# Kernel tuning notes

Hardware: AMD Instinct MI355X
Metric: run time of the kernel (lower is better)

Reference implementation:

```python
import jax, jax.numpy as jnp
import numpy as np

EMBED_DIM = 512
N_HEADS = 16
HEAD_DIM = EMBED_DIM // N_HEADS  # 32


def setup_inputs() -> dict:
    key0 = jax.random.key(0)
    ks = jax.random.split(key0, 8)
    B, S, D = 4, 2048, EMBED_DIM
    inp = {
        "key": jax.random.normal(ks[0], (B, S, D), dtype=jnp.float32),
        "query": jax.random.normal(ks[1], (B, S, D), dtype=jnp.float32),
        "value": jax.random.normal(ks[2], (B, S, D), dtype=jnp.float32),
        # per-head projection weights (nn.Linear: y = x @ W.T), no bias
        "Wq": jax.random.normal(ks[3], (HEAD_DIM, HEAD_DIM), dtype=jnp.float32) * 0.1,
        "Wk": jax.random.normal(ks[4], (HEAD_DIM, HEAD_DIM), dtype=jnp.float32) * 0.1,
        "Wv": jax.random.normal(ks[5], (HEAD_DIM, HEAD_DIM), dtype=jnp.float32) * 0.1,
        # output projection with bias
        "Wo": jax.random.normal(ks[6], (EMBED_DIM, EMBED_DIM), dtype=jnp.float32) * 0.05,
        "bo": jax.random.normal(ks[7], (EMBED_DIM,), dtype=jnp.float32) * 0.01,
    }
    return inp


def reference(key, query, value, Wq, Wk, Wv, Wo, bo):
    B, S, D = key.shape
    Sq = query.shape[1]
    H, dh = N_HEADS, HEAD_DIM
    # reshape to [B, S, H, dh] then per-head linear (x @ W.T)
    k = jnp.einsum('bshd,ed->bhse', key.reshape(B, S, H, dh), Wk)
    q = jnp.einsum('bshd,ed->bhse', query.reshape(B, Sq, H, dh), Wq)
    v = jnp.einsum('bshd,ed->bhse', value.reshape(B, S, H, dh), Wv)
    # naive attention: full [B,H,Sq,S] scores
    scores = jnp.einsum('bhqd,bhkd->bhqk', q, k) / jnp.sqrt(jnp.float32(dh))
    attn = jax.nn.softmax(scores, axis=-1)
    ctx = jnp.einsum('bhqk,bhkd->bhqd', attn, v)  # [B,H,Sq,dh]
    concat = ctx.transpose(0, 2, 1, 3).reshape(B, Sq, H * dh)
    return concat @ Wo.T + bo
```

## Files before the change

kernel.cpp:

```cpp
#include <hip/hip_runtime.h>
#include <hip/hip_bf16.h>


typedef __attribute__((ext_vector_type(8))) short bf16x8;
typedef __attribute__((ext_vector_type(4))) float f32x4;

#define MFMA16(a, b, c) __builtin_amdgcn_mfma_f32_16x16x32_bf16(a, b, c, 0, 0, 0)

static __device__ __forceinline__ unsigned short f2bf(float f) {
  __bf16 h = (__bf16)f;
  union { __bf16 h; unsigned short u; } c; c.h = h; return c.u;
}
static __device__ __forceinline__ float bf2f(unsigned short u) {
  union { unsigned u; float f; } c; c.u = ((unsigned)u) << 16; return c.f;
}

static __device__ __forceinline__ void gld_lds16(const ushort* g, ushort* l) {
  __builtin_amdgcn_global_load_lds(
      (const __attribute__((address_space(1))) unsigned int*)g,
      (__attribute__((address_space(3))) unsigned int*)l, 16, 0, 0);
}

static __device__ __forceinline__ void load8_split(const float* p, bf16x8& hi, bf16x8& lo) {
  float4 a = *(const float4*)p;
  float4 b = *(const float4*)(p + 4);
  float v[8] = {a.x, a.y, a.z, a.w, b.x, b.y, b.z, b.w};
  #pragma unroll
  for (int j = 0; j < 8; ++j) {
    unsigned short h = f2bf(v[j]);
    hi[j] = (short)h;
    lo[j] = (short)f2bf(v[j] - bf2f(h));
  }
}

__global__ __launch_bounds__(256) void proj_kernel(
    const float* __restrict__ key, const float* __restrict__ query,
    const float* __restrict__ value,
    const float* __restrict__ Wq, const float* __restrict__ Wk,
    const float* __restrict__ Wv, const float* __restrict__ Wo,
    ushort* __restrict__ Qp, ushort* __restrict__ Kp, ushort* __restrict__ Vt,
    ushort* __restrict__ Wob) {
  if (blockIdx.x >= 2048) {
    int i = ((blockIdx.x - 2048) * 256 + threadIdx.x) * 4;
    float4 v = *(const float4*)&Wo[i];
    ushort4 o;
    o.x = f2bf(v.x); o.y = f2bf(v.y); o.z = f2bf(v.z); o.w = f2bf(v.w);
    *(ushort4*)&Wob[i] = o;
    return;
  }
  __shared__ ushort tlds[4][16][40];
  const int tid = threadIdx.x;
  const int l = tid & 63, wid = tid >> 6;
  const int lr = l & 15, lc = l >> 4;
  const int task = blockIdx.x * 4 + wid;
  const int h = task & 15;
  const int st = (task >> 4) & 127;
  const int b = task >> 11;
  const int bh = b * 16 + h;
  const size_t xoff = ((size_t)b * 2048 + st * 16 + lr) * 512 + h * 32 + lc * 8;
  const float ALPHA = 0.2550354039f;

  #pragma unroll
  for (int t = 0; t < 3; ++t) {
    const float* x = (t == 0) ? query : (t == 1) ? key : value;
    const float* W = (t == 0) ? Wq : (t == 1) ? Wk : Wv;
    bf16x8 xh, xl;
    load8_split(x + xoff, xh, xl);
    f32x4 accs[2];
    #pragma unroll
    for (int eh = 0; eh < 2; ++eh) {
      bf16x8 wh, wl;
      load8_split(W + (size_t)(eh * 16 + lr) * 32 + lc * 8, wh, wl);
      f32x4 acc = {0.f, 0.f, 0.f, 0.f};
      acc = MFMA16(xh, wh, acc);
      acc = MFMA16(xh, wl, acc);
      acc = MFMA16(xl, wh, acc);
      accs[eh] = acc;
    }
    if (t == 2) {
      #pragma unroll
      for (int eh = 0; eh < 2; ++eh) {
        ushort4 pk;
        pk.x = f2bf(accs[eh][0]); pk.y = f2bf(accs[eh][1]);
        pk.z = f2bf(accs[eh][2]); pk.w = f2bf(accs[eh][3]);
        *(ushort4*)&Vt[((size_t)bh * 32 + eh * 16 + lr) * 2048 + st * 16 + lc * 4] = pk;
      }
    } else {
      const float scale = (t == 0) ? ALPHA : 1.0f;
      #pragma unroll
      for (int eh = 0; eh < 2; ++eh)
        #pragma unroll
        for (int r = 0; r < 4; ++r)
          tlds[wid][lc * 4 + r][eh * 16 + lr] = f2bf(accs[eh][r] * scale);
      bf16x8 row = *(const bf16x8*)&tlds[wid][l >> 2][(l & 3) * 8];
      ushort* dst = ((t == 0) ? Qp : Kp) +
                    ((size_t)bh * 2048 + st * 16 + (l >> 2)) * 32 + (l & 3) * 8;
      *(bf16x8*)dst = row;
    }
  }
}

__global__ __launch_bounds__(256) void attn_kernel(
    const ushort* __restrict__ Qp, const ushort* __restrict__ Kp,
    const ushort* __restrict__ Vt, ushort* __restrict__ Cb) {
  __shared__ ushort plds[4][16][68];
  __shared__ ushort kbuf[3][2048];
  __shared__ ushort vbuf[3][2048];
  const int tid = threadIdx.x;
  const int l = tid & 63, w = tid >> 6;
  const int lr = l & 15, lc = l >> 4;
  const int xcd = blockIdx.x & 7, idx = blockIdx.x >> 3;
  const int bh = xcd * 8 + (idx >> 4);
  const int qblk = idx & 15;
  const int b = bh >> 4, h = bh & 15;
  const int q0 = qblk * 128 + w * 32;

  const ushort* Qb = Qp + (size_t)bh * 2048 * 32;
  const ushort* Kb = Kp + (size_t)bh * 2048 * 32;
  const ushort* Vb = Vt + (size_t)bh * 32 * 2048;

  const int sig = tid ^ ((tid >> 3) & 7);
  const ushort* kg_src = Kb + (size_t)sig * 8;
  const ushort* vg_src = Vb + (size_t)(tid >> 3) * 2048 +
                         (((tid & 7) ^ ((tid >> 3) & 7)) * 8);

  int koff[4];
  #pragma unroll
  for (int kg = 0; kg < 4; ++kg) {
    int v = (kg * 16 + lr) * 4 + lc;
    v ^= (v >> 3) & 7;
    koff[kg] = v * 8;
  }
  int voff[2][2];
  #pragma unroll
  for (int kc = 0; kc < 2; ++kc)
    #pragma unroll
    for (int eh = 0; eh < 2; ++eh) {
      int v = (eh * 16 + lr) * 8 + kc * 4 + lc;
      v ^= (v >> 3) & 7;
      voff[kc][eh] = v * 8;
    }

  bf16x8 qf[2];
  qf[0] = *(const bf16x8*)&Qb[(size_t)(q0 + lr) * 32 + lc * 8];
  qf[1] = *(const bf16x8*)&Qb[(size_t)(q0 + 16 + lr) * 32 + lc * 8];

  bf16x8 ones;
  #pragma unroll
  for (int j = 0; j < 8; ++j) ones[j] = (short)0x3F80;

  f32x4 octx[2][2] = {};
  f32x4 dacc[2] = {};
  const f32x4 zero = {0.f, 0.f, 0.f, 0.f};

  gld_lds16(kg_src, &kbuf[0][tid * 8]);
  gld_lds16(vg_src, &vbuf[0][tid * 8]);
  gld_lds16(kg_src + (size_t)64 * 32, &kbuf[1][tid * 8]);
  gld_lds16(vg_src + 64, &vbuf[1][tid * 8]);
  asm volatile("s_waitcnt vmcnt(2)" ::: "memory");
  __builtin_amdgcn_s_barrier();

  int cur = 0, nx2 = 2;
  for (int kt = 0; kt < 32; ++kt) {
    if (kt < 30) {
      const int k0n = (kt + 2) * 64;
      gld_lds16(kg_src + (size_t)k0n * 32, &kbuf[nx2][tid * 8]);
      gld_lds16(vg_src + k0n, &vbuf[nx2][tid * 8]);
    }

    const ushort* kb = kbuf[cur];
    const ushort* vb = vbuf[cur];
    bf16x8 kf[4];
    #pragma unroll
    for (int kg = 0; kg < 4; ++kg)
      kf[kg] = *(const bf16x8*)&kb[koff[kg]];
    bf16x8 vf[2][2];
    #pragma unroll
    for (int kc = 0; kc < 2; ++kc)
      #pragma unroll
      for (int eh = 0; eh < 2; ++eh)
        vf[kc][eh] = *(const bf16x8*)&vb[voff[kc][eh]];

    #pragma unroll
    for (int qi = 0; qi < 2; ++qi) {
      f32x4 sc[4];
      #pragma unroll
      for (int kg = 0; kg < 4; ++kg)
        sc[kg] = MFMA16(kf[kg], qf[qi], zero);
      #pragma unroll
      for (int kg = 0; kg < 4; ++kg) {
        float p0 = __builtin_amdgcn_exp2f(sc[kg][0]);
        float p1 = __builtin_amdgcn_exp2f(sc[kg][1]);
        float p2 = __builtin_amdgcn_exp2f(sc[kg][2]);
        float p3 = __builtin_amdgcn_exp2f(sc[kg][3]);
        ushort4 pk;
        pk.x = f2bf(p0); pk.y = f2bf(p1); pk.z = f2bf(p2); pk.w = f2bf(p3);
        *(ushort4*)&plds[w][lr][kg * 16 + lc * 4] = pk;
      }
      #pragma unroll
      for (int kc = 0; kc < 2; ++kc) {
        union { ushort4 q[2]; bf16x8 v; } u;
        u.q[0] = *(const ushort4*)&plds[w][lr][kc * 32 + lc * 8];
        u.q[1] = *(const ushort4*)&plds[w][lr][kc * 32 + lc * 8 + 4];
        #pragma unroll
        for (int eh = 0; eh < 2; ++eh)
          octx[qi][eh] = MFMA16(u.v, vf[kc][eh], octx[qi][eh]);
        dacc[qi] = MFMA16(u.v, ones, dacc[qi]);
      }
    }

    if (kt < 30) {
      asm volatile("s_waitcnt vmcnt(2)" ::: "memory");
    } else {
      asm volatile("s_waitcnt vmcnt(0)" ::: "memory");
    }
    __builtin_amdgcn_s_barrier();
    cur = (cur == 2) ? 0 : cur + 1;
    nx2 = (nx2 == 2) ? 0 : nx2 + 1;
  }

  #pragma unroll
  for (int qi = 0; qi < 2; ++qi) {
    float inv[4];
    #pragma unroll
    for (int r = 0; r < 4; ++r)
      inv[r] = 1.0f / dacc[qi][r];
    #pragma unroll
    for (int eh = 0; eh < 2; ++eh)
      #pragma unroll
      for (int r = 0; r < 4; ++r) {
        float v = octx[qi][eh][r] * inv[r];
        Cb[((size_t)b * 2048 + q0 + qi * 16 + lc * 4 + r) * 512 + h * 32 + eh * 16 + lr] =
            f2bf(v);
      }
  }
}

__global__ __launch_bounds__(256) void oproj_kernel(
    const ushort* __restrict__ Cb, const ushort* __restrict__ Wob,
    const float* __restrict__ bo, float* __restrict__ out) {
  const int tid = threadIdx.x;
  const int l = tid & 63, w = tid >> 6;
  const int lr = l & 15, lc = l >> 4;
  const int qt = blockIdx.x >> 1;
  const int nt = blockIdx.x & 1;
  const int r0 = qt * 64;
  const int n0 = nt * 256 + w * 64;

  f32x4 acc[4][4] = {};
  for (int kk = 0; kk < 16; ++kk) {
    const int k0 = kk * 32;
    bf16x8 af[4], bf[4];
    #pragma unroll
    for (int i = 0; i < 4; ++i)
      af[i] = *(const bf16x8*)&Cb[(size_t)(r0 + i * 16 + lr) * 512 + k0 + lc * 8];
    #pragma unroll
    for (int j = 0; j < 4; ++j)
      bf[j] = *(const bf16x8*)&Wob[(size_t)(n0 + j * 16 + lr) * 512 + k0 + lc * 8];
    #pragma unroll
    for (int i = 0; i < 4; ++i)
      #pragma unroll
      for (int j = 0; j < 4; ++j)
        acc[i][j] = MFMA16(af[i], bf[j], acc[i][j]);
  }
  #pragma unroll
  for (int j = 0; j < 4; ++j) {
    float bias = bo[n0 + j * 16 + lr];
    #pragma unroll
    for (int i = 0; i < 4; ++i)
      #pragma unroll
      for (int r = 0; r < 4; ++r)
        out[(size_t)(r0 + i * 16 + lc * 4 + r) * 512 + n0 + j * 16 + lr] =
            acc[i][j][r] + bias;
  }
}

extern "C" void kernel_launch(void* const* d_in, const int* in_sizes, int n_in,
                              void* d_out, int out_size, void* d_ws, size_t ws_size,
                              hipStream_t stream) {
  (void)in_sizes; (void)n_in; (void)out_size; (void)ws_size;
  const float* key   = (const float*)d_in[0];
  const float* query = (const float*)d_in[1];
  const float* value = (const float*)d_in[2];
  const float* Wq    = (const float*)d_in[3];
  const float* Wk    = (const float*)d_in[4];
  const float* Wv    = (const float*)d_in[5];
  const float* Wo    = (const float*)d_in[6];
  const float* bo    = (const float*)d_in[7];
  float* out = (float*)d_out;

  const size_t NT = (size_t)4 * 16 * 2048 * 32;
  ushort* ws  = (ushort*)d_ws;
  ushort* Qp  = ws;
  ushort* Kp  = Qp + NT;
  ushort* Vt  = Kp + NT;
  ushort* Cb  = Vt + NT;
  ushort* Wob = Cb + NT;

  hipLaunchKernelGGL(proj_kernel, dim3(2304), dim3(256), 0, stream,
                     key, query, value, Wq, Wk, Wv, Wo, Qp, Kp, Vt, Wob);
  hipLaunchKernelGGL(attn_kernel, dim3(1024), dim3(256), 0, stream, Qp, Kp, Vt, Cb);
  hipLaunchKernelGGL(oproj_kernel, dim3(256), dim3(256), 0, stream, Cb, Wob, bo, out);
}
```

Before: 102.6 us.

## Permute K tile load order so softmax probabilities feed PV MFMA from registers

Reorders the rows of each K tile as they are loaded into shared memory, so that the score MFMA output layout directly matches the A-operand layout needed by the P·V MFMA. This removes the per-wave shared-memory staging buffer for probabilities, along with its write and read-back. The exp2 and bf16 conversion now happen in registers right before each PV MFMA. The risk is a wrong permutation, which would misalign keys with values, and a possible change in register pressure.

```diff
diff --git a/kernel.cpp b/kernel.cpp
--- a/kernel.cpp
+++ b/kernel.cpp
@@ -103,24 +103,25 @@
 __global__ __launch_bounds__(256) void attn_kernel(
     const ushort* __restrict__ Qp, const ushort* __restrict__ Kp,
     const ushort* __restrict__ Vt, ushort* __restrict__ Cb) {
-  __shared__ ushort plds[4][16][68];
   __shared__ ushort kbuf[3][2048];
   __shared__ ushort vbuf[3][2048];
   const int tid = threadIdx.x;
-  const int l = tid & 63, w = tid >> 6;
+  const int l = tid & 63;
   const int lr = l & 15, lc = l >> 4;
   const int xcd = blockIdx.x & 7, idx = blockIdx.x >> 3;
   const int bh = xcd * 8 + (idx >> 4);
   const int qblk = idx & 15;
   const int b = bh >> 4, h = bh & 15;
-  const int q0 = qblk * 128 + w * 32;
+  const int q0 = qblk * 128 + (tid >> 6) * 32;
 
   const ushort* Qb = Qp + (size_t)bh * 2048 * 32;
   const ushort* Kb = Kp + (size_t)bh * 2048 * 32;
   const ushort* Vb = Vt + (size_t)bh * 32 * 2048;
 
-  const int sig = tid ^ ((tid >> 3) & 7);
-  const ushort* kg_src = Kb + (size_t)sig * 8;
+  const int s = tid ^ ((tid >> 3) & 7);
+  const int m = s >> 2, pp = s & 3;
+  const int g = (m & 32) | ((m & 12) << 1) | ((m & 16) >> 2) | (m & 3);
+  const ushort* kg_src = Kb + (size_t)(g * 4 + pp) * 8;
   const ushort* vg_src = Vb + (size_t)(tid >> 3) * 2048 +
                          (((tid & 7) ^ ((tid >> 3) & 7)) * 8);
 
@@ -188,24 +189,17 @@
       for (int kg = 0; kg < 4; ++kg)
         sc[kg] = MFMA16(kf[kg], qf[qi], zero);
       #pragma unroll
-      for (int kg = 0; kg < 4; ++kg) {
-        float p0 = __builtin_amdgcn_exp2f(sc[kg][0]);
-        float p1 = __builtin_amdgcn_exp2f(sc[kg][1]);
-        float p2 = __builtin_amdgcn_exp2f(sc[kg][2]);
-        float p3 = __builtin_amdgcn_exp2f(sc[kg][3]);
-        ushort4 pk;
-        pk.x = f2bf(p0); pk.y = f2bf(p1); pk.z = f2bf(p2); pk.w = f2bf(p3);
-        *(ushort4*)&plds[w][lr][kg * 16 + lc * 4] = pk;
-      }
-      #pragma unroll
       for (int kc = 0; kc < 2; ++kc) {
-        union { ushort4 q[2]; bf16x8 v; } u;
-        u.q[0] = *(const ushort4*)&plds[w][lr][kc * 32 + lc * 8];
-        u.q[1] = *(const ushort4*)&plds[w][lr][kc * 32 + lc * 8 + 4];
+        bf16x8 pa;
+        #pragma unroll
+        for (int r = 0; r < 4; ++r) {
+          pa[r]     = (short)f2bf(__builtin_amdgcn_exp2f(sc[2 * kc][r]));
+          pa[4 + r] = (short)f2bf(__builtin_amdgcn_exp2f(sc[2 * kc + 1][r]));
+        }
         #pragma unroll
         for (int eh = 0; eh < 2; ++eh)
-          octx[qi][eh] = MFMA16(u.v, vf[kc][eh], octx[qi][eh]);
-        dacc[qi] = MFMA16(u.v, ones, dacc[qi]);
+          octx[qi][eh] = MFMA16(pa, vf[kc][eh], octx[qi][eh]);
+        dacc[qi] = MFMA16(pa, ones, dacc[qi]);
       }
     }
 
```

New measurement: 98.49 us. -4.0%, faster.
